# Performance work log

Hardware: AMD Instinct MI355X
Metric: run time of the kernel (lower is better)

Reference implementation:

```python
import jax, jax.numpy as jnp
import numpy as np

N = 2_097_152          # sampled points
H = 16                 # hash heads / levels
F = 2                  # features per head
M = 524_288            # 2**19 table size
HID = 64               # mlp width
OUT = 3


def setup_inputs() -> dict:
    key = jax.random.key(0)
    ks = jax.random.split(key, 12)
    idx = jax.random.randint(ks[0], (N, H), 0, M, dtype=jnp.int64)
    tables = jax.random.normal(ks[1], (H, M, F), dtype=jnp.float32) * 0.02
    d_in = H * F  # 32
    def lin(k, d1, d2):
        kw, kb = jax.random.split(k)
        s = 1.0 / np.sqrt(d1)
        W = jax.random.uniform(kw, (d1, d2), jnp.float32, -s, s)
        b = jax.random.uniform(kb, (d2,), jnp.float32, -s, s)
        return W, b
    W1, b1 = lin(ks[2], d_in, HID)
    W2, b2 = lin(ks[3], HID, HID)
    W3, b3 = lin(ks[4], HID, HID)
    W4, b4 = lin(ks[5], HID, OUT)
    return {"idx": idx, "tables": tables,
            "W1": W1, "b1": b1, "W2": W2, "b2": b2,
            "W3": W3, "b3": b3, "W4": W4, "b4": b4}


def reference(idx, tables, W1, b1, W2, b2, W3, b3, W4, b4):
    # per-head gather: tables[h][idx[:, h]] -> [N, H, F], then concat heads
    gather = jax.vmap(lambda t, i: t[i], in_axes=(0, 1), out_axes=1)
    x = gather(tables, idx).reshape(idx.shape[0], -1)  # [N, H*F]
    x = jax.nn.relu(x @ W1 + b1)
    x = jax.nn.relu(x @ W2 + b2)
    x = jax.nn.relu(x @ W3 + b3)
    return x @ W4 + b4  # [N, 3]
```

## Files before the change

### kernel.cpp

```cpp
#include <hip/hip_runtime.h>
#include <hip/hip_bf16.h>

typedef __attribute__((ext_vector_type(8))) short short8;
typedef __attribute__((ext_vector_type(4))) float floatx4;
typedef __attribute__((ext_vector_type(4))) int int4v;
typedef __attribute__((ext_vector_type(4))) unsigned int uint4v;

#define MTBL 524288
#define HSTRIDE 72

union U4S8 { uint4v u; short8 s; };

static __device__ __forceinline__ unsigned int pack2bf(float a, float b) {
    union { float f; unsigned int u; } x, y;
    x.f = a; y.f = b;
    unsigned int lo = (x.u + 0x8000u) >> 16;
    unsigned int hi = (y.u + 0x8000u) & 0xFFFF0000u;
    return lo | hi;
}
static __device__ __forceinline__ short bf1(float a) {
    union { float f; unsigned int u; } x;
    x.f = a;
    return (short)((x.u + 0x8000u) >> 16);
}

static __device__ __forceinline__ short8 relu_pack(floatx4 a, floatx4 b) {
    U4S8 r;
    r.u[0] = pack2bf(fmaxf(a[0], 0.f), fmaxf(a[1], 0.f));
    r.u[1] = pack2bf(fmaxf(a[2], 0.f), fmaxf(a[3], 0.f));
    r.u[2] = pack2bf(fmaxf(b[0], 0.f), fmaxf(b[1], 0.f));
    r.u[3] = pack2bf(fmaxf(b[2], 0.f), fmaxf(b[3], 0.f));
    return r.s;
}

__global__ __launch_bounds__(256) void ngp_prep(
    const int* __restrict__ idx, int* __restrict__ idxT,
    const floatx4* __restrict__ tab4, unsigned int* __restrict__ tblC, int N)
{
    const int tblocks = N >> 10;
    if ((int)blockIdx.x < tblocks) {
        const int t  = blockIdx.x * 256 + threadIdx.x;
        const int p0 = t * 4;
        const int4v* rows = (const int4v*)idx;
        int4v r[4][4];
#pragma unroll
        for (int p = 0; p < 4; ++p)
#pragma unroll
            for (int c = 0; c < 4; ++c)
                r[p][c] = __builtin_nontemporal_load(rows + (size_t)(p0 + p) * 4 + c);
#pragma unroll
        for (int c = 0; c < 4; ++c)
#pragma unroll
            for (int k = 0; k < 4; ++k) {
                const int h = c * 4 + k;
                int4v w;
                w[0] = r[0][c][k]; w[1] = r[1][c][k]; w[2] = r[2][c][k]; w[3] = r[3][c][k];
                __builtin_nontemporal_store(w, (int4v*)(idxT + (size_t)h * N + p0));
            }
    } else {
        const int t = (blockIdx.x - tblocks) * 256 + threadIdx.x;
        floatx4 a = __builtin_nontemporal_load(tab4 + (size_t)2 * t);
        floatx4 b = __builtin_nontemporal_load(tab4 + (size_t)2 * t + 1);
        uint4v w;
        w[0] = pack2bf(a[0], a[1]);
        w[1] = pack2bf(a[2], a[3]);
        w[2] = pack2bf(b[0], b[1]);
        w[3] = pack2bf(b[2], b[3]);
        __builtin_nontemporal_store(w, (uint4v*)(tblC + (size_t)4 * t));
    }
}

__global__ __launch_bounds__(256) void ngp_gather_ph(
    const int* __restrict__ idxT, const unsigned int* __restrict__ tblC,
    unsigned int* __restrict__ xU, int N, int phase, int iters)
{
    const int h    = ((blockIdx.x & 7) << 1) | phase;
    const int slot = blockIdx.x >> 3;
    const int* __restrict__ ih = idxT + (size_t)h * N;
    const unsigned int* __restrict__ th = tblC + (size_t)h * MTBL;
    unsigned int* __restrict__ xh = xU + (size_t)h * N;

    int p = slot * (N >> 8) + (threadIdx.x << 3);
    int4v iv0 = __builtin_nontemporal_load((const int4v*)(ih + p));
    int4v iv1 = __builtin_nontemporal_load((const int4v*)(ih + p + 4));
    for (int it = 0; it < iters; ++it) {
        int4v nv0, nv1;
        if (it + 1 < iters) {
            nv0 = __builtin_nontemporal_load((const int4v*)(ih + p + 2048));
            nv1 = __builtin_nontemporal_load((const int4v*)(ih + p + 2052));
        }
        uint4v w0, w1;
        w0[0] = th[iv0[0]]; w0[1] = th[iv0[1]]; w0[2] = th[iv0[2]]; w0[3] = th[iv0[3]];
        w1[0] = th[iv1[0]]; w1[1] = th[iv1[1]]; w1[2] = th[iv1[2]]; w1[3] = th[iv1[3]];
        __builtin_nontemporal_store(w0, (uint4v*)(xh + p));
        __builtin_nontemporal_store(w1, (uint4v*)(xh + p + 4));
        iv0 = nv0; iv1 = nv1;
        p += 2048;
    }
}

__global__ __launch_bounds__(256, 2) void ngp_mlp(
    const unsigned int* __restrict__ xU,
    const float* __restrict__ W1, const float* __restrict__ b1,
    const float* __restrict__ W2, const float* __restrict__ b2,
    const float* __restrict__ W3, const float* __restrict__ b3,
    const float* __restrict__ W4, const float* __restrict__ b4,
    float* __restrict__ out, int N, int tiles_per_wave)
{
    __shared__ float sW[10632];

    const int tid  = threadIdx.x;
    for (int i = tid; i < 2048; i += 256) sW[i] = W1[i];
    for (int i = tid; i < 4096; i += 256) sW[2048 + i] = W2[i];
    for (int i = tid; i < 4096; i += 256) sW[6144 + i] = W3[i];
    if (tid < 192) sW[10240 + tid] = W4[tid];
    if (tid < 64)       sW[10432 + tid] = b1[tid];
    else if (tid < 128) sW[10432 + tid] = b2[tid - 64];
    else if (tid < 192) sW[10432 + tid] = b3[tid - 128];
    else if (tid < 195) sW[10432 + tid] = b4[tid - 192];
    __syncthreads();

    const int wave = tid >> 6;
    const int lane = tid & 63;
    const int q = lane >> 4;
    const int m = lane & 15;

    int ct[4];
#pragma unroll
    for (int t = 0; t < 4; ++t)
        ct[t] = 32 * (t >> 1) + 4 * (t & 1) + 8 * (m >> 2) + (m & 3);

    short8 A1[4], A2[4][2], A3[4][2], A4[2];
    floatx4 C1[4], C2[4], C3[4], C4;

#pragma unroll
    for (int t = 0; t < 4; ++t) {
        short8 a;
#pragma unroll
        for (int j = 0; j < 8; ++j)
            a[j] = bf1(sW[(q * 8 + j) * 64 + ct[t]]);
        A1[t] = a;
    }
#pragma unroll
    for (int t = 0; t < 4; ++t)
#pragma unroll
        for (int c = 0; c < 2; ++c) {
            short8 a2, a3;
#pragma unroll
            for (int j = 0; j < 8; ++j) {
                a2[j] = bf1(sW[2048 + (c * 32 + q * 8 + j) * 64 + ct[t]]);
                a3[j] = bf1(sW[6144 + (c * 32 + q * 8 + j) * 64 + ct[t]]);
            }
            A2[t][c] = a2;
            A3[t][c] = a3;
        }
#pragma unroll
    for (int c = 0; c < 2; ++c) {
        short8 a;
#pragma unroll
        for (int j = 0; j < 8; ++j)
            a[j] = (m < 3) ? bf1(sW[10240 + (c * 32 + q * 8 + j) * 3 + m]) : (short)0;
        A4[c] = a;
    }
#pragma unroll
    for (int t = 0; t < 4; ++t) {
        const int bi = 32 * (t >> 1) + 4 * (t & 1) + 8 * q;
#pragma unroll
        for (int r = 0; r < 4; ++r) {
            C1[t][r] = sW[10432 + bi + r];
            C2[t][r] = sW[10432 + 64 + bi + r];
            C3[t][r] = sW[10432 + 128 + bi + r];
        }
    }
#pragma unroll
    for (int r = 0; r < 4; ++r)
        C4[r] = (q == 0 && r < 3) ? sW[10432 + 192 + r] : 0.0f;

    const int gw = blockIdx.x * 4 + wave;
    const int tile0 = gw * tiles_per_wave;

    const unsigned int* xr = xU + (size_t)(q * 4) * N + m;

    uint4v cur;
    {
        const int c0 = tile0 * 16;
        cur[0] = xr[c0];
        cur[1] = xr[(size_t)N + c0];
        cur[2] = xr[(size_t)2 * N + c0];
        cur[3] = xr[(size_t)3 * N + c0];
    }

    for (int it = 0; it < tiles_per_wave; ++it) {
        const int pbase = (tile0 + it) * 16;
        const bool more = (it + 1) < tiles_per_wave;

        U4S8 bx; bx.u = cur;
        const short8 Bx = bx.s;

        uint4v nxt;
        if (more) {
            const int cn = pbase + 16;
            nxt[0] = xr[cn];
            nxt[1] = xr[(size_t)N + cn];
            nxt[2] = xr[(size_t)2 * N + cn];
            nxt[3] = xr[(size_t)3 * N + cn];
        }

        floatx4 h1[4];
#pragma unroll
        for (int t = 0; t < 4; ++t)
            h1[t] = __builtin_amdgcn_mfma_f32_16x16x32_bf16(A1[t], Bx, C1[t], 0, 0, 0);

        short8 B0 = relu_pack(h1[0], h1[1]);
        short8 B1 = relu_pack(h1[2], h1[3]);

        floatx4 h2[4];
#pragma unroll
        for (int t = 0; t < 4; ++t) {
            h2[t] = __builtin_amdgcn_mfma_f32_16x16x32_bf16(A2[t][0], B0, C2[t], 0, 0, 0);
            h2[t] = __builtin_amdgcn_mfma_f32_16x16x32_bf16(A2[t][1], B1, h2[t], 0, 0, 0);
        }
        B0 = relu_pack(h2[0], h2[1]);
        B1 = relu_pack(h2[2], h2[3]);

        floatx4 h3[4];
#pragma unroll
        for (int t = 0; t < 4; ++t) {
            h3[t] = __builtin_amdgcn_mfma_f32_16x16x32_bf16(A3[t][0], B0, C3[t], 0, 0, 0);
            h3[t] = __builtin_amdgcn_mfma_f32_16x16x32_bf16(A3[t][1], B1, h3[t], 0, 0, 0);
        }
        B0 = relu_pack(h3[0], h3[1]);
        B1 = relu_pack(h3[2], h3[3]);

        floatx4 o;
        o = __builtin_amdgcn_mfma_f32_16x16x32_bf16(A4[0], B0, C4, 0, 0, 0);
        o = __builtin_amdgcn_mfma_f32_16x16x32_bf16(A4[1], B1, o, 0, 0, 0);

        if (q == 0) {
            const int pn = pbase + m;
            out[pn * 3 + 0] = o[0];
            out[pn * 3 + 1] = o[1];
            out[pn * 3 + 2] = o[2];
        }

        cur = nxt;
    }
}

__global__ __launch_bounds__(256, 2) void ngp_fused(
    const int* __restrict__ idx,
    const float* __restrict__ tables,
    const float* __restrict__ W1, const float* __restrict__ b1,
    const float* __restrict__ W2, const float* __restrict__ b2,
    const float* __restrict__ W3, const float* __restrict__ b3,
    const float* __restrict__ W4, const float* __restrict__ b4,
    float* __restrict__ out, int tiles_per_wave)
{
    __shared__ float sW1[2048];
    __shared__ float sW2[4096];
    __shared__ float sW3[4096];
    __shared__ float sW4[192];
    __shared__ float sB[200];
    __shared__ __hip_bfloat16 sH[4][16 * HSTRIDE];

    const int tid = threadIdx.x;
    for (int i = tid; i < 2048; i += 256) sW1[i] = W1[i];
    for (int i = tid; i < 4096; i += 256) sW2[i] = W2[i];
    for (int i = tid; i < 4096; i += 256) sW3[i] = W3[i];
    if (tid < 192) sW4[tid] = W4[tid];
    if (tid < 64)       sB[tid] = b1[tid];
    else if (tid < 128) sB[tid] = b2[tid - 64];
    else if (tid < 192) sB[tid] = b3[tid - 128];
    else if (tid < 195) sB[tid] = b4[tid - 192];
    __syncthreads();

    const int wave = tid >> 6;
    const int lane = tid & 63;
    const int q = lane >> 4;
    const int m = lane & 15;

    short8 A1[4], A2[4][2], A3[4][2], A4[2];
#pragma unroll
    for (int t = 0; t < 4; ++t) {
        short8 a;
#pragma unroll
        for (int j = 0; j < 8; ++j)
            a[j] = bf1(sW1[(q * 8 + j) * 64 + t * 16 + m]);
        A1[t] = a;
    }
#pragma unroll
    for (int t = 0; t < 4; ++t)
#pragma unroll
        for (int c = 0; c < 2; ++c) {
            short8 a, a3;
#pragma unroll
            for (int j = 0; j < 8; ++j) {
                a[j]  = bf1(sW2[(c * 32 + q * 8 + j) * 64 + t * 16 + m]);
                a3[j] = bf1(sW3[(c * 32 + q * 8 + j) * 64 + t * 16 + m]);
            }
            A2[t][c] = a;
            A3[t][c] = a3;
        }
#pragma unroll
    for (int c = 0; c < 2; ++c) {
        short8 a;
#pragma unroll
        for (int j = 0; j < 8; ++j)
            a[j] = (m < 3) ? bf1(sW4[(c * 32 + q * 8 + j) * 3 + m]) : (short)0;
        A4[c] = a;
    }

    floatx4 C1[4], C2[4], C3[4], C4;
#pragma unroll
    for (int t = 0; t < 4; ++t)
#pragma unroll
        for (int r = 0; r < 4; ++r) {
            C1[t][r] = sB[t * 16 + q * 4 + r];
            C2[t][r] = sB[64 + t * 16 + q * 4 + r];
            C3[t][r] = sB[128 + t * 16 + q * 4 + r];
        }
#pragma unroll
    for (int r = 0; r < 4; ++r)
        C4[r] = (q == 0 && r < 3) ? sB[192 + r] : 0.0f;

    __hip_bfloat16* hrow = &sH[wave][m * HSTRIDE];
    const int4*   idx4 = (const int4*)idx;
    const float2* tbl  = (const float2*)tables;

    const int gw = blockIdx.x * 4 + wave;
    const int tile0 = gw * tiles_per_wave;

    int4 iv = idx4[(tile0 * 16 + m) * 4 + q];
    float2 g0 = tbl[(q * 4 + 0) * MTBL + iv.x];
    float2 g1 = tbl[(q * 4 + 1) * MTBL + iv.y];
    float2 g2 = tbl[(q * 4 + 2) * MTBL + iv.z];
    float2 g3 = tbl[(q * 4 + 3) * MTBL + iv.w];

    for (int it = 0; it < tiles_per_wave; ++it) {
        const int pbase = (tile0 + it) * 16;
        const bool more = (it + 1) < tiles_per_wave;

        short8 Bx;
        {
            unsigned int p0 = pack2bf(g0.x, g0.y);
            unsigned int p1 = pack2bf(g1.x, g1.y);
            unsigned int p2 = pack2bf(g2.x, g2.y);
            unsigned int p3 = pack2bf(g3.x, g3.y);
            Bx[0] = (short)(p0 & 0xFFFF); Bx[1] = (short)(p0 >> 16);
            Bx[2] = (short)(p1 & 0xFFFF); Bx[3] = (short)(p1 >> 16);
            Bx[4] = (short)(p2 & 0xFFFF); Bx[5] = (short)(p2 >> 16);
            Bx[6] = (short)(p3 & 0xFFFF); Bx[7] = (short)(p3 >> 16);
        }

        int4 ivn;
        if (more) ivn = idx4[((pbase + 16) + m) * 4 + q];

        floatx4 acc[4];
#pragma unroll
        for (int t = 0; t < 4; ++t)
            acc[t] = __builtin_amdgcn_mfma_f32_16x16x32_bf16(A1[t], Bx, C1[t], 0, 0, 0);

#pragma unroll
        for (int t = 0; t < 4; ++t) {
            uint2 pk;
            pk.x = pack2bf(fmaxf(acc[t][0], 0.f), fmaxf(acc[t][1], 0.f));
            pk.y = pack2bf(fmaxf(acc[t][2], 0.f), fmaxf(acc[t][3], 0.f));
            *(uint2*)(hrow + t * 16 + q * 4) = pk;
        }
        short8 Bh0 = *(const short8*)(hrow + q * 8);
        short8 Bh1 = *(const short8*)(hrow + 32 + q * 8);

#pragma unroll
        for (int t = 0; t < 4; ++t) {
            acc[t] = __builtin_amdgcn_mfma_f32_16x16x32_bf16(A2[t][0], Bh0, C2[t], 0, 0, 0);
            acc[t] = __builtin_amdgcn_mfma_f32_16x16x32_bf16(A2[t][1], Bh1, acc[t], 0, 0, 0);
        }

        if (more) {
            g0 = tbl[(q * 4 + 0) * MTBL + ivn.x];
            g1 = tbl[(q * 4 + 1) * MTBL + ivn.y];
            g2 = tbl[(q * 4 + 2) * MTBL + ivn.z];
            g3 = tbl[(q * 4 + 3) * MTBL + ivn.w];
        }

#pragma unroll
        for (int t = 0; t < 4; ++t) {
            uint2 pk;
            pk.x = pack2bf(fmaxf(acc[t][0], 0.f), fmaxf(acc[t][1], 0.f));
            pk.y = pack2bf(fmaxf(acc[t][2], 0.f), fmaxf(acc[t][3], 0.f));
            *(uint2*)(hrow + t * 16 + q * 4) = pk;
        }
        Bh0 = *(const short8*)(hrow + q * 8);
        Bh1 = *(const short8*)(hrow + 32 + q * 8);

#pragma unroll
        for (int t = 0; t < 4; ++t) {
            acc[t] = __builtin_amdgcn_mfma_f32_16x16x32_bf16(A3[t][0], Bh0, C3[t], 0, 0, 0);
            acc[t] = __builtin_amdgcn_mfma_f32_16x16x32_bf16(A3[t][1], Bh1, acc[t], 0, 0, 0);
        }

#pragma unroll
        for (int t = 0; t < 4; ++t) {
            uint2 pk;
            pk.x = pack2bf(fmaxf(acc[t][0], 0.f), fmaxf(acc[t][1], 0.f));
            pk.y = pack2bf(fmaxf(acc[t][2], 0.f), fmaxf(acc[t][3], 0.f));
            *(uint2*)(hrow + t * 16 + q * 4) = pk;
        }
        Bh0 = *(const short8*)(hrow + q * 8);
        Bh1 = *(const short8*)(hrow + 32 + q * 8);

        floatx4 o;
        o = __builtin_amdgcn_mfma_f32_16x16x32_bf16(A4[0], Bh0, C4, 0, 0, 0);
        o = __builtin_amdgcn_mfma_f32_16x16x32_bf16(A4[1], Bh1, o, 0, 0, 0);

        if (q == 0) {
            const int pn = pbase + m;
            out[pn * 3 + 0] = o[0];
            out[pn * 3 + 1] = o[1];
            out[pn * 3 + 2] = o[2];
        }
    }
}

extern "C" void kernel_launch(void* const* d_in, const int* in_sizes, int n_in,
                              void* d_out, int out_size, void* d_ws, size_t ws_size,
                              hipStream_t stream) {
    const int*   idx    = (const int*)d_in[0];
    const float* tables = (const float*)d_in[1];
    const float* W1 = (const float*)d_in[2];
    const float* b1 = (const float*)d_in[3];
    const float* W2 = (const float*)d_in[4];
    const float* b2 = (const float*)d_in[5];
    const float* W3 = (const float*)d_in[6];
    const float* b3 = (const float*)d_in[7];
    const float* W4 = (const float*)d_in[8];
    const float* b4 = (const float*)d_in[9];
    float* out = (float*)d_out;

    const int N = in_sizes[0] / 16;
    const int total_tiles = N / 16;

    const size_t idxT_bytes = (size_t)16 * N * 4;
    const size_t xU_bytes   = (size_t)16 * N * 4;
    const size_t tblC_bytes = (size_t)16 * MTBL * 4;
    const size_t need = idxT_bytes + xU_bytes + tblC_bytes;

    if (ws_size >= need) {
        int*          idxT = (int*)d_ws;
        unsigned int* xU   = (unsigned int*)((char*)d_ws + idxT_bytes);
        unsigned int* tblC = (unsigned int*)((char*)d_ws + idxT_bytes + xU_bytes);

        const int tblocks = N / 1024;
        const int cblocks = (16 * MTBL) / 1024;
        ngp_prep<<<tblocks + cblocks, 256, 0, stream>>>(
            idx, idxT, (const floatx4*)tables, tblC, N);
        const int iters = (N >> 8) >> 11;
        ngp_gather_ph<<<2048, 256, 0, stream>>>(idxT, tblC, xU, N, 0, iters);
        ngp_gather_ph<<<2048, 256, 0, stream>>>(idxT, tblC, xU, N, 1, iters);
        const int blocks = 2048;
        const int tiles_per_wave = total_tiles / (blocks * 4);
        ngp_mlp<<<blocks, 256, 0, stream>>>(xU, W1, b1, W2, b2, W3, b3, W4, b4,
                                            out, N, tiles_per_wave);
    } else {
        const int blocks = 2048;
        const int tiles_per_wave = total_tiles / (blocks * 4);
        ngp_fused<<<blocks, 256, 0, stream>>>(idx, tables, W1, b1, W2, b2, W3, b3,
                                              W4, b4, out, tiles_per_wave);
    }
}
```

Before: 632.4 us.

## Fuse hash gather into MLP kernel, dropping index transpose and staging buffer

Replaces the four-kernel pipeline (prep with index transpose, two per-head gather passes, then MLP) with a bf16 table compression kernel plus one fused kernel. The fused kernel reads idx rows directly, gathers packed features from the compressed tables, and feeds them to the MFMA MLP chain, processing two tiles per iteration with software-prefetched indices and gathers. This removes the idxT and xU round-trips through HBM and two launches. The cost is that random table gathers now happen inside the MLP kernel, so their latency must be hidden by the prefetch, and the kernel may need more registers.

New measurement: 759.8 us. +20.2%, slower.

```diff
diff --git a/kernel.cpp b/kernel.cpp
--- a/kernel.cpp
+++ b/kernel.cpp
@@ -33,83 +33,82 @@
     return r.s;
 }
 
-__global__ __launch_bounds__(256) void ngp_prep(
-    const int* __restrict__ idx, int* __restrict__ idxT,
-    const floatx4* __restrict__ tab4, unsigned int* __restrict__ tblC, int N)
+__global__ __launch_bounds__(256) void ngp_compress(
+    const floatx4* __restrict__ tab4, unsigned int* __restrict__ tblC)
 {
-    const int tblocks = N >> 10;
-    if ((int)blockIdx.x < tblocks) {
-        const int t  = blockIdx.x * 256 + threadIdx.x;
-        const int p0 = t * 4;
-        const int4v* rows = (const int4v*)idx;
-        int4v r[4][4];
-#pragma unroll
-        for (int p = 0; p < 4; ++p)
-#pragma unroll
-            for (int c = 0; c < 4; ++c)
-                r[p][c] = __builtin_nontemporal_load(rows + (size_t)(p0 + p) * 4 + c);
-#pragma unroll
-        for (int c = 0; c < 4; ++c)
-#pragma unroll
-            for (int k = 0; k < 4; ++k) {
-                const int h = c * 4 + k;
-                int4v w;
-                w[0] = r[0][c][k]; w[1] = r[1][c][k]; w[2] = r[2][c][k]; w[3] = r[3][c][k];
-                __builtin_nontemporal_store(w, (int4v*)(idxT + (size_t)h * N + p0));
-            }
-    } else {
-        const int t = (blockIdx.x - tblocks) * 256 + threadIdx.x;
-        floatx4 a = __builtin_nontemporal_load(tab4 + (size_t)2 * t);
-        floatx4 b = __builtin_nontemporal_load(tab4 + (size_t)2 * t + 1);
-        uint4v w;
-        w[0] = pack2bf(a[0], a[1]);
-        w[1] = pack2bf(a[2], a[3]);
-        w[2] = pack2bf(b[0], b[1]);
-        w[3] = pack2bf(b[2], b[3]);
-        __builtin_nontemporal_store(w, (uint4v*)(tblC + (size_t)4 * t));
-    }
-}
-
-__global__ __launch_bounds__(256) void ngp_gather_ph(
-    const int* __restrict__ idxT, const unsigned int* __restrict__ tblC,
-    unsigned int* __restrict__ xU, int N, int phase, int iters)
+    const int t = blockIdx.x * 256 + threadIdx.x;
+    floatx4 a = __builtin_nontemporal_load(tab4 + (size_t)2 * t);
+    floatx4 b = __builtin_nontemporal_load(tab4 + (size_t)2 * t + 1);
+    uint4v w;
+    w[0] = pack2bf(a[0], a[1]);
+    w[1] = pack2bf(a[2], a[3]);
+    w[2] = pack2bf(b[0], b[1]);
+    w[3] = pack2bf(b[2], b[3]);
+    __builtin_nontemporal_store(w, (uint4v*)(tblC + (size_t)4 * t));
+}
+
+static __device__ __forceinline__ uint4v gather4(
+    const unsigned int* __restrict__ tq, int4v iv)
 {
-    const int h    = ((blockIdx.x & 7) << 1) | phase;
-    const int slot = blockIdx.x >> 3;
-    const int* __restrict__ ih = idxT + (size_t)h * N;
-    const unsigned int* __restrict__ th = tblC + (size_t)h * MTBL;
-    unsigned int* __restrict__ xh = xU + (size_t)h * N;
-
-    int p = slot * (N >> 8) + (threadIdx.x << 3);
-    int4v iv0 = __builtin_nontemporal_load((const int4v*)(ih + p));
-    int4v iv1 = __builtin_nontemporal_load((const int4v*)(ih + p + 4));
-    for (int it = 0; it < iters; ++it) {
-        int4v nv0, nv1;
-        if (it + 1 < iters) {
-            nv0 = __builtin_nontemporal_load((const int4v*)(ih + p + 2048));
-            nv1 = __builtin_nontemporal_load((const int4v*)(ih + p + 2052));
-        }
-        uint4v w0, w1;
-        w0[0] = th[iv0[0]]; w0[1] = th[iv0[1]]; w0[2] = th[iv0[2]]; w0[3] = th[iv0[3]];
-        w1[0] = th[iv1[0]]; w1[1] = th[iv1[1]]; w1[2] = th[iv1[2]]; w1[3] = th[iv1[3]];
-        __builtin_nontemporal_store(w0, (uint4v*)(xh + p));
-        __builtin_nontemporal_store(w1, (uint4v*)(xh + p + 4));
-        iv0 = nv0; iv1 = nv1;
-        p += 2048;
-    }
-}
-
-__global__ __launch_bounds__(256, 2) void ngp_mlp(
-    const unsigned int* __restrict__ xU,
+    uint4v g;
+    g[0] = tq[iv[0]];
+    g[1] = tq[MTBL + iv[1]];
+    g[2] = tq[(size_t)2 * MTBL + iv[2]];
+    g[3] = tq[(size_t)3 * MTBL + iv[3]];
+    return g;
+}
+
+static __device__ __forceinline__ floatx4 mlp_chain(
+    uint4v cur,
+    const short8 (&A1)[4], const short8 (&A2)[4][2], const short8 (&A3)[4][2],
+    const short8 (&A4)[2],
+    const floatx4 (&C1)[4], const floatx4 (&C2)[4], const floatx4 (&C3)[4],
+    floatx4 C4)
+{
+    U4S8 bx; bx.u = cur;
+    const short8 Bx = bx.s;
+
+    floatx4 h[4];
+#pragma unroll
+    for (int t = 0; t < 4; ++t)
+        h[t] = __builtin_amdgcn_mfma_f32_16x16x32_bf16(A1[t], Bx, C1[t], 0, 0, 0);
+    short8 B0 = relu_pack(h[0], h[1]);
+    short8 B1 = relu_pack(h[2], h[3]);
+
+#pragma unroll
+    for (int t = 0; t < 4; ++t) {
+        h[t] = __builtin_amdgcn_mfma_f32_16x16x32_bf16(A2[t][0], B0, C2[t], 0, 0, 0);
+        h[t] = __builtin_amdgcn_mfma_f32_16x16x32_bf16(A2[t][1], B1, h[t], 0, 0, 0);
+    }
+    B0 = relu_pack(h[0], h[1]);
+    B1 = relu_pack(h[2], h[3]);
+
+#pragma unroll
+    for (int t = 0; t < 4; ++t) {
+        h[t] = __builtin_amdgcn_mfma_f32_16x16x32_bf16(A3[t][0], B0, C3[t], 0, 0, 0);
+        h[t] = __builtin_amdgcn_mfma_f32_16x16x32_bf16(A3[t][1], B1, h[t], 0, 0, 0);
+    }
+    B0 = relu_pack(h[0], h[1]);
+    B1 = relu_pack(h[2], h[3]);
+
+    floatx4 o;
+    o = __builtin_amdgcn_mfma_f32_16x16x32_bf16(A4[0], B0, C4, 0, 0, 0);
+    o = __builtin_amdgcn_mfma_f32_16x16x32_bf16(A4[1], B1, o, 0, 0, 0);
+    return o;
+}
+
+__global__ __launch_bounds__(256, 2) void ngp_fused2(
+    const int* __restrict__ idx,
+    const unsigned int* __restrict__ tblC,
     const float* __restrict__ W1, const float* __restrict__ b1,
     const float* __restrict__ W2, const float* __restrict__ b2,
     const float* __restrict__ W3, const float* __restrict__ b3,
     const float* __restrict__ W4, const float* __restrict__ b4,
-    float* __restrict__ out, int N, int tiles_per_wave)
+    float* __restrict__ out, int tiles_per_wave)
 {
     __shared__ float sW[10632];
 
-    const int tid  = threadIdx.x;
+    const int tid = threadIdx.x;
     for (int i = tid; i < 2048; i += 256) sW[i] = W1[i];
     for (int i = tid; i < 4096; i += 256) sW[2048 + i] = W2[i];
     for (int i = tid; i < 4096; i += 256) sW[6144 + i] = W3[i];
@@ -178,73 +177,55 @@
 
     const int gw = blockIdx.x * 4 + wave;
     const int tile0 = gw * tiles_per_wave;
-
-    const unsigned int* xr = xU + (size_t)(q * 4) * N + m;
-
-    uint4v cur;
-    {
-        const int c0 = tile0 * 16;
-        cur[0] = xr[c0];
-        cur[1] = xr[(size_t)N + c0];
-        cur[2] = xr[(size_t)2 * N + c0];
-        cur[3] = xr[(size_t)3 * N + c0];
-    }
-
-    for (int it = 0; it < tiles_per_wave; ++it) {
-        const int pbase = (tile0 + it) * 16;
-        const bool more = (it + 1) < tiles_per_wave;
-
-        U4S8 bx; bx.u = cur;
-        const short8 Bx = bx.s;
-
-        uint4v nxt;
+    const int iters = tiles_per_wave >> 1;
+
+    const int4v* __restrict__ idx4 = (const int4v*)idx;
+    const unsigned int* __restrict__ tq = tblC + (size_t)(q * 4) * MTBL;
+
+    #define IDXLD(t) __builtin_nontemporal_load(idx4 + (size_t)((t) * 16 + m) * 4 + q)
+
+    int4v ivA = IDXLD(tile0);
+    int4v ivB = IDXLD(tile0 + 1);
+    uint4v curA = gather4(tq, ivA);
+    uint4v curB = gather4(tq, ivB);
+    if (iters > 1) {
+        ivA = IDXLD(tile0 + 2);
+        ivB = IDXLD(tile0 + 3);
+    }
+
+    for (int k = 0; k < iters; ++k) {
+        const int pbaseA = (tile0 + 2 * k) * 16;
+        const bool more  = (k + 1) < iters;
+        const bool more2 = (k + 2) < iters;
+
+        uint4v nxtA = curA, nxtB = curB;
         if (more) {
-            const int cn = pbase + 16;
-            nxt[0] = xr[cn];
-            nxt[1] = xr[(size_t)N + cn];
-            nxt[2] = xr[(size_t)2 * N + cn];
-            nxt[3] = xr[(size_t)3 * N + cn];
-        }
-
-        floatx4 h1[4];
-#pragma unroll
-        for (int t = 0; t < 4; ++t)
-            h1[t] = __builtin_amdgcn_mfma_f32_16x16x32_bf16(A1[t], Bx, C1[t], 0, 0, 0);
-
-        short8 B0 = relu_pack(h1[0], h1[1]);
-        short8 B1 = relu_pack(h1[2], h1[3]);
-
-        floatx4 h2[4];
-#pragma unroll
-        for (int t = 0; t < 4; ++t) {
-            h2[t] = __builtin_amdgcn_mfma_f32_16x16x32_bf16(A2[t][0], B0, C2[t], 0, 0, 0);
-            h2[t] = __builtin_amdgcn_mfma_f32_16x16x32_bf16(A2[t][1], B1, h2[t], 0, 0, 0);
-        }
-        B0 = relu_pack(h2[0], h2[1]);
-        B1 = relu_pack(h2[2], h2[3]);
-
-        floatx4 h3[4];
-#pragma unroll
-        for (int t = 0; t < 4; ++t) {
-            h3[t] = __builtin_amdgcn_mfma_f32_16x16x32_bf16(A3[t][0], B0, C3[t], 0, 0, 0);
-            h3[t] = __builtin_amdgcn_mfma_f32_16x16x32_bf16(A3[t][1], B1, h3[t], 0, 0, 0);
-        }
-        B0 = relu_pack(h3[0], h3[1]);
-        B1 = relu_pack(h3[2], h3[3]);
-
-        floatx4 o;
-        o = __builtin_amdgcn_mfma_f32_16x16x32_bf16(A4[0], B0, C4, 0, 0, 0);
-        o = __builtin_amdgcn_mfma_f32_16x16x32_bf16(A4[1], B1, o, 0, 0, 0);
+            nxtA = gather4(tq, ivA);
+            nxtB = gather4(tq, ivB);
+        }
+        if (more2) {
+            ivA = IDXLD(tile0 + 2 * k + 4);
+            ivB = IDXLD(tile0 + 2 * k + 5);
+        }
+
+        floatx4 oA = mlp_chain(curA, A1, A2, A3, A4, C1, C2, C3, C4);
+        floatx4 oB = mlp_chain(curB, A1, A2, A3, A4, C1, C2, C3, C4);
 
         if (q == 0) {
-            const int pn = pbase + m;
-            out[pn * 3 + 0] = o[0];
-            out[pn * 3 + 1] = o[1];
-            out[pn * 3 + 2] = o[2];
-        }
-
-        cur = nxt;
-    }
+            const int pA = pbaseA + m;
+            __builtin_nontemporal_store(oA[0], out + pA * 3 + 0);
+            __builtin_nontemporal_store(oA[1], out + pA * 3 + 1);
+            __builtin_nontemporal_store(oA[2], out + pA * 3 + 2);
+            const int pB = pA + 16;
+            __builtin_nontemporal_store(oB[0], out + pB * 3 + 0);
+            __builtin_nontemporal_store(oB[1], out + pB * 3 + 1);
+            __builtin_nontemporal_store(oB[2], out + pB * 3 + 2);
+        }
+
+        curA = nxtA;
+        curB = nxtB;
+    }
+    #undef IDXLD
 }
 
 __global__ __launch_bounds__(256, 2) void ngp_fused(
@@ -439,28 +420,18 @@
 
     const int N = in_sizes[0] / 16;
     const int total_tiles = N / 16;
-
-    const size_t idxT_bytes = (size_t)16 * N * 4;
-    const size_t xU_bytes   = (size_t)16 * N * 4;
     const size_t tblC_bytes = (size_t)16 * MTBL * 4;
-    const size_t need = idxT_bytes + xU_bytes + tblC_bytes;
-
-    if (ws_size >= need) {
-        int*          idxT = (int*)d_ws;
-        unsigned int* xU   = (unsigned int*)((char*)d_ws + idxT_bytes);
-        unsigned int* tblC = (unsigned int*)((char*)d_ws + idxT_bytes + xU_bytes);
-
-        const int tblocks = N / 1024;
-        const int cblocks = (16 * MTBL) / 1024;
-        ngp_prep<<<tblocks + cblocks, 256, 0, stream>>>(
-            idx, idxT, (const floatx4*)tables, tblC, N);
-        const int iters = (N >> 8) >> 11;
-        ngp_gather_ph<<<2048, 256, 0, stream>>>(idxT, tblC, xU, N, 0, iters);
-        ngp_gather_ph<<<2048, 256, 0, stream>>>(idxT, tblC, xU, N, 1, iters);
+
+    if (ws_size >= tblC_bytes) {
+        unsigned int* tblC = (unsigned int*)d_ws;
+
+        ngp_compress<<<(16 * MTBL) / 1024, 256, 0, stream>>>(
+            (const floatx4*)tables, tblC);
         const int blocks = 2048;
         const int tiles_per_wave = total_tiles / (blocks * 4);
-        ngp_mlp<<<blocks, 256, 0, stream>>>(xU, W1, b1, W2, b2, W3, b3, W4, b4,
-                                            out, N, tiles_per_wave);
+        ngp_fused2<<<blocks, 256, 0, stream>>>(idx, tblC, W1, b1, W2, b2,
+                                               W3, b3, W4, b4, out,
+                                               tiles_per_wave);
     } else {
         const int blocks = 2048;
         const int tiles_per_wave = total_tiles / (blocks * 4);
```
